# Optimization experiments

Hardware: AMD Instinct MI355X
Metric: run time of the kernel (lower is better)

Reference implementation:

```python
import jax, jax.numpy as jnp
import numpy as np

B, T, D = 2, 1024, 2048      # batch, seq, model dim
E, F, K = 64, 512, 4          # n_experts, expert hidden, top-k
S, HS = 2, 512 * 4            # shared experts, shared hidden = expert_dim * topk


def setup_inputs() -> dict:
    key = jax.random.key(0)
    ks = jax.random.split(key, 9)
    s = 0.02
    f32 = jnp.float32
    return {
        "x": jax.random.normal(ks[0], (B, T, D), f32),
        "router_w": jax.random.normal(ks[1], (D, E), f32) * s,
        "router_bias": jnp.zeros((E,), f32),
        "wg": jax.random.normal(ks[2], (E, D, F), f32) * s,
        "wu": jax.random.normal(ks[3], (E, D, F), f32) * s,
        "wd": jax.random.normal(ks[4], (E, F, D), f32) * s,
        "swg": jax.random.normal(ks[5], (S, D, HS), f32) * s,
        "swu": jax.random.normal(ks[6], (S, D, HS), f32) * s,
        "swd": jax.random.normal(ks[7], (S, HS, D), f32) * s,
    }


def reference(x, router_w, router_bias, wg, wu, wd, swg, swu, swd):
    b, t, d = x.shape
    flat = x.reshape(b * t, d)                      # [N, D]
    n = flat.shape[0]

    # Router: softmax scores, top-k selection on (logits + bias)
    logits = flat @ router_w                         # [N, E]
    scores = jax.nn.softmax(logits, axis=-1)
    _, topk_idx = jax.lax.top_k(logits + router_bias, K)          # [N, K]
    topk_scores = jnp.take_along_axis(scores, topk_idx, axis=-1)  # [N, K]
    topk_scores = topk_scores / topk_scores.sum(axis=-1, keepdims=True)

    # Dense combine weights: w[n, e] = normalized score if expert e selected else 0
    comb = jnp.zeros((n, E), dtype=flat.dtype).at[
        jnp.arange(n)[:, None], topk_idx].set(topk_scores)        # [N, E]

    # Routed experts (SwiGLU), computed densely and masked by combine weights
    g = jax.nn.silu(jnp.einsum('nd,edf->nef', flat, wg))          # [N, E, F]
    u = jnp.einsum('nd,edf->nef', flat, wu)                       # [N, E, F]
    routed = jnp.einsum('ne,nef,efd->nd', comb, g * u, wd)        # [N, D]

    # Shared experts (always active, summed)
    sg = jax.nn.silu(jnp.einsum('nd,sdh->nsh', flat, swg))        # [N, S, HS]
    su = jnp.einsum('nd,sdh->nsh', flat, swu)
    shared = jnp.einsum('nsh,shd->nd', sg * su, swd)              # [N, D]

    return (routed + shared).reshape(b, t, d)
```

## Files before the change

kernel.cpp:

```cpp
#include <hip/hip_runtime.h>
#include <hip/hip_bf16.h>

typedef __bf16 bf16x8 __attribute__((ext_vector_type(8)));
typedef float f32x4 __attribute__((ext_vector_type(4)));
typedef unsigned short u16x4 __attribute__((ext_vector_type(4)));
typedef unsigned short u16x8 __attribute__((ext_vector_type(8)));

#define DEVI __device__ __forceinline__

constexpr int N_TOK = 2048;
constexpr int DIM   = 2048;
constexpr int NEXP  = 64;
constexpr int FDIM  = 512;
constexpr int TOPK  = 4;
constexpr int NSH   = 2;
constexpr int HSH   = 2048;

constexpr int BM = 128, BN = 128, BK = 64, KS = 8;

DEVI unsigned short f2b(float f) {
  union { float fv; unsigned u; } v; v.fv = f;
  unsigned r = v.u + 0x7fffu + ((v.u >> 16) & 1u);
  return (unsigned short)(r >> 16);
}
DEVI float b2f(unsigned short h) {
  union { unsigned u; float f; } v; v.u = ((unsigned)h) << 16;
  return v.f;
}
DEVI void gll16(const void* g, void* l) {
  __builtin_amdgcn_global_load_lds((const __attribute__((address_space(1))) unsigned*)g,
                                   (__attribute__((address_space(3))) unsigned*)l, 16, 0, 0);
}

__global__ void cvt_x_kernel(const float* __restrict__ x, unsigned short* __restrict__ xb) {
  const size_t i = ((size_t)blockIdx.x * 256 + threadIdx.x) * 8;
  const float4 a = *reinterpret_cast<const float4*>(x + i);
  const float4 b = *reinterpret_cast<const float4*>(x + i + 4);
  u16x8 o;
  o[0] = f2b(a.x); o[1] = f2b(a.y); o[2] = f2b(a.z); o[3] = f2b(a.w);
  o[4] = f2b(b.x); o[5] = f2b(b.y); o[6] = f2b(b.z); o[7] = f2b(b.w);
  *reinterpret_cast<u16x8*>(xb + i) = o;
}

__global__ __launch_bounds__(256)
void tr_shared_kernel(const float* __restrict__ swu, const float* __restrict__ swg,
                      const float* __restrict__ swd, unsigned short* __restrict__ swuT,
                      unsigned short* __restrict__ swgT, unsigned short* __restrict__ swdT) {
  __shared__ float Lf[64][68];
  const int tid = threadIdx.x;
  const int r0 = blockIdx.x * 64, c0 = blockIdx.y * 64;
  const int z = blockIdx.z, mat = z >> 1;
  const size_t soff = (size_t)(z & 1) * DIM * HSH;
  const float* in = (mat == 0 ? swu : mat == 1 ? swg : swd) + soff;
  unsigned short* ot = (mat == 0 ? swuT : mat == 1 ? swgT : swdT) + soff;
  #pragma unroll
  for (int j = 0; j < 4; ++j) {
    const int idx = j * 1024 + tid * 4;
    const int row = idx >> 6, col = idx & 63;
    const float4 v = *reinterpret_cast<const float4*>(in + (size_t)(r0 + row) * 2048 + c0 + col);
    *reinterpret_cast<float4*>(&Lf[row][col]) = v;
  }
  __syncthreads();
  #pragma unroll
  for (int j = 0; j < 4; ++j) {
    const int idx = j * 1024 + tid * 4;
    const int orow = idx >> 6, ocol = idx & 63;
    u16x4 o;
    o[0] = f2b(Lf[ocol][orow]);     o[1] = f2b(Lf[ocol + 1][orow]);
    o[2] = f2b(Lf[ocol + 2][orow]); o[3] = f2b(Lf[ocol + 3][orow]);
    *reinterpret_cast<u16x4*>(ot + (size_t)(c0 + orow) * 2048 + r0 + ocol) = o;
  }
}

__global__ void router_kernel(const float* __restrict__ x, const float* __restrict__ rw,
                              const float* __restrict__ rb, int* __restrict__ cnt,
                              int* __restrict__ listTok, float* __restrict__ listW) {
  const int lane = threadIdx.x & 63;
  const int wave = threadIdx.x >> 6;
  const int tokBase = blockIdx.x * 8 + wave * 2;
  const float* __restrict__ xr0 = x + (size_t)tokBase * DIM;
  const float* __restrict__ xr1 = xr0 + DIM;
  float acc0 = 0.f, acc1 = 0.f;
  for (int d = 0; d < DIM; ++d) {
    const float r = rw[(size_t)d * NEXP + lane];
    acc0 = fmaf(xr0[d], r, acc0);
    acc1 = fmaf(xr1[d], r, acc1);
  }
  const float bias = rb[lane];
  #pragma unroll
  for (int t = 0; t < 2; ++t) {
    const float v = (t == 0) ? acc0 : acc1;
    const int token = tokBase + t;
    float m = v;
    #pragma unroll
    for (int o = 32; o > 0; o >>= 1) m = fmaxf(m, __shfl_xor(m, o));
    const float p = expf(v - m);
    float ss = p;
    #pragma unroll
    for (int o = 32; o > 0; o >>= 1) ss += __shfl_xor(ss, o);
    const float score = p / ss;
    float cur = v + bias;
    float wk[TOPK]; int ik[TOPK]; float wsum = 0.f;
    #pragma unroll
    for (int k = 0; k < TOPK; ++k) {
      float tm = cur;
      #pragma unroll
      for (int o = 32; o > 0; o >>= 1) tm = fmaxf(tm, __shfl_xor(tm, o));
      const unsigned long long msk = __ballot(cur == tm);
      const int sel = (int)__builtin_ctzll(msk);
      const float w = __shfl(score, sel);
      wk[k] = w; ik[k] = sel; wsum += w;
      if (lane == sel) cur = -3.4e38f;
    }
    if (lane < TOPK) {
      const int e = ik[lane];
      const float w = wk[lane] / wsum;
      const int slot = atomicAdd(&cnt[e], 1);
      listTok[(size_t)e * N_TOK + slot] = token;
      listW[(size_t)e * N_TOK + slot] = w;
    }
  }
}

__global__ void scan_kernel(const int* __restrict__ cnt, int* __restrict__ off) {
  if (threadIdx.x == 0) {
    int s = 0;
    for (int e = 0; e < NEXP; ++e) { off[e] = s; s += cnt[e]; }
  }
}

template<bool ROUTED>
__global__ __launch_bounds__(256, 2)
void up_fused_kernel(const unsigned short* __restrict__ xb,
                     const float* __restrict__ Wu, const float* __restrict__ Wg,
                     const unsigned short* __restrict__ WuT, const unsigned short* __restrict__ WgT,
                     const int* __restrict__ cnt, const int* __restrict__ off,
                     const int* __restrict__ listTok, const float* __restrict__ listW,
                     unsigned short* __restrict__ H) {
  const int Ftot = ROUTED ? FDIM : HSH;
  const int tid = threadIdx.x;
  const int f0 = blockIdx.x * BN;
  const int e  = blockIdx.y;
  const int m0 = blockIdx.z * BM;
  int rcnt, rowbase;
  if (ROUTED) {
    const int c = cnt[e];
    if (m0 >= c) return;
    rcnt = min(BM, c - m0);
    rowbase = off[e] + m0;
  } else {
    rcnt = BM;
    rowbase = e * N_TOK + m0;
  }

  __shared__ __align__(16) unsigned short Al[KS][BM][8];
  __shared__ __align__(16) unsigned short Bu[KS][BN][8];
  __shared__ __align__(16) unsigned short Bg[KS][BN][8];
  __shared__ int tokS[BM];
  __shared__ float wS[BM];

  if (tid < BM) {
    if (ROUTED) {
      const bool v = tid < rcnt;
      tokS[tid] = listTok[(size_t)e * N_TOK + m0 + (v ? tid : 0)];
      wS[tid]   = v ? listW[(size_t)e * N_TOK + m0 + tid] : 0.f;
    } else { tokS[tid] = m0 + tid; wS[tid] = 1.f; }
  }
  __syncthreads();

  const int wid = tid >> 6, l = tid & 63;
  const int wm = wid >> 1, wn = wid & 1;
  const int lc = l & 15, hi = l >> 4;

  const unsigned short* pa0 = xb + (size_t)tokS[l] * DIM;
  const unsigned short* pa1 = xb + (size_t)tokS[64 + l] * DIM;

  const unsigned short *pbu0 = nullptr, *pbu1 = nullptr, *pbg0 = nullptr, *pbg1 = nullptr;
  if constexpr (!ROUTED) {
    const unsigned short* wut = WuT + (size_t)e * HSH * DIM;
    const unsigned short* wgt = WgT + (size_t)e * HSH * DIM;
    pbu0 = wut + (size_t)(f0 + l) * DIM;  pbu1 = wut + (size_t)(f0 + 64 + l) * DIM;
    pbg0 = wgt + (size_t)(f0 + l) * DIM;  pbg1 = wgt + (size_t)(f0 + 64 + l) * DIM;
  }
  const int bf = tid & 127, kh = tid >> 7;
  const float *wpu = nullptr, *wpg = nullptr;
  if constexpr (ROUTED) {
    wpu = Wu + (size_t)e * DIM * FDIM + (size_t)(kh * 32) * FDIM + f0 + bf;
    wpg = Wg + (size_t)e * DIM * FDIM + (size_t)(kh * 32) * FDIM + f0 + bf;
  }
  unsigned short* bdstU = &Bu[kh * 4][bf][0];
  unsigned short* bdstG = &Bg[kh * 4][bf][0];

  f32x4 au[4][4], ag[4][4];
  #pragma unroll
  for (int i = 0; i < 4; ++i)
    #pragma unroll
    for (int j = 0; j < 4; ++j) { au[i][j] = f32x4{0,0,0,0}; ag[i][j] = f32x4{0,0,0,0}; }

  for (int d0 = 0; d0 < DIM; d0 += BK) {
    gll16(pa0 + d0 + (2 * wid) * 8,     &Al[2 * wid][0][0]);
    gll16(pa1 + d0 + (2 * wid) * 8,     &Al[2 * wid][64][0]);
    gll16(pa0 + d0 + (2 * wid + 1) * 8, &Al[2 * wid + 1][0][0]);
    gll16(pa1 + d0 + (2 * wid + 1) * 8, &Al[2 * wid + 1][64][0]);
    if constexpr (!ROUTED) {
      gll16(pbu0 + d0 + (2 * wid) * 8,     &Bu[2 * wid][0][0]);
      gll16(pbu1 + d0 + (2 * wid) * 8,     &Bu[2 * wid][64][0]);
      gll16(pbu0 + d0 + (2 * wid + 1) * 8, &Bu[2 * wid + 1][0][0]);
      gll16(pbu1 + d0 + (2 * wid + 1) * 8, &Bu[2 * wid + 1][64][0]);
      gll16(pbg0 + d0 + (2 * wid) * 8,     &Bg[2 * wid][0][0]);
      gll16(pbg1 + d0 + (2 * wid) * 8,     &Bg[2 * wid][64][0]);
      gll16(pbg0 + d0 + (2 * wid + 1) * 8, &Bg[2 * wid + 1][0][0]);
      gll16(pbg1 + d0 + (2 * wid + 1) * 8, &Bg[2 * wid + 1][64][0]);
    } else {
      float r[32];
      #pragma unroll
      for (int j = 0; j < 32; ++j) r[j] = wpu[(size_t)(d0 + j) * FDIM];
      #pragma unroll
      for (int jg = 0; jg < 4; ++jg) {
        u16x8 pk;
        #pragma unroll
        for (int q = 0; q < 8; ++q) pk[q] = f2b(r[jg * 8 + q]);
        *reinterpret_cast<u16x8*>(bdstU + jg * BN * 8) = pk;
      }
      #pragma unroll
      for (int j = 0; j < 32; ++j) r[j] = wpg[(size_t)(d0 + j) * FDIM];
      #pragma unroll
      for (int jg = 0; jg < 4; ++jg) {
        u16x8 pk;
        #pragma unroll
        for (int q = 0; q < 8; ++q) pk[q] = f2b(r[jg * 8 + q]);
        *reinterpret_cast<u16x8*>(bdstG + jg * BN * 8) = pk;
      }
    }
    __syncthreads();
    #pragma unroll
    for (int ks = 0; ks < 2; ++ks) {
      bf16x8 af[4], bu_[4], bg_[4];
      #pragma unroll
      for (int i = 0; i < 4; ++i)
        af[i] = *reinterpret_cast<const bf16x8*>(&Al[ks * 4 + hi][wm * 64 + i * 16 + lc][0]);
      #pragma unroll
      for (int i = 0; i < 4; ++i) {
        bu_[i] = *reinterpret_cast<const bf16x8*>(&Bu[ks * 4 + hi][wn * 64 + i * 16 + lc][0]);
        bg_[i] = *reinterpret_cast<const bf16x8*>(&Bg[ks * 4 + hi][wn * 64 + i * 16 + lc][0]);
      }
      #pragma unroll
      for (int mi = 0; mi < 4; ++mi)
        #pragma unroll
        for (int ni = 0; ni < 4; ++ni) {
          au[mi][ni] = __builtin_amdgcn_mfma_f32_16x16x32_bf16(af[mi], bu_[ni], au[mi][ni], 0, 0, 0);
          ag[mi][ni] = __builtin_amdgcn_mfma_f32_16x16x32_bf16(af[mi], bg_[ni], ag[mi][ni], 0, 0, 0);
        }
    }
    __syncthreads();
  }

  #pragma unroll
  for (int mi = 0; mi < 4; ++mi)
    #pragma unroll
    for (int ni = 0; ni < 4; ++ni)
      #pragma unroll
      for (int r2 = 0; r2 < 4; ++r2) {
        const int row = wm * 64 + mi * 16 + hi * 4 + r2;
        if (row < rcnt) {
          const int col = f0 + wn * 64 + ni * 16 + lc;
          const float g = ag[mi][ni][r2], u = au[mi][ni][r2];
          const float h = (g / (1.f + __expf(-g))) * u * wS[row];
          H[(size_t)(rowbase + row) * Ftot + col] = f2b(h);
        }
      }
}

__global__ __launch_bounds__(256, 2)
void down_kernel(const unsigned short* __restrict__ Hr, const unsigned short* __restrict__ Hs,
                 const float* __restrict__ wd, const unsigned short* __restrict__ swdT,
                 const int* __restrict__ cnt, const int* __restrict__ off,
                 const int* __restrict__ listTok, float* __restrict__ out) {
  const int tid = threadIdx.x;
  const int x0 = blockIdx.x * BN;
  const int y  = blockIdx.y;
  const int m0 = blockIdx.z * BM;
  const bool routed = y < NEXP;
  int rcnt, Kd;
  const unsigned short* Ab;
  const float* wb = nullptr;
  const unsigned short* wbT = nullptr;

  __shared__ int tokS[BM];
  __shared__ __align__(16) unsigned short Al[KS][BM][8];
  __shared__ __align__(16) unsigned short Bl[KS][BN][8];

  if (routed) {
    const int c = cnt[y];
    if (m0 >= c) return;
    rcnt = min(BM, c - m0); Kd = FDIM;
    Ab = Hr + (size_t)(off[y] + m0) * FDIM;
    wb = wd + (size_t)y * FDIM * DIM;
    if (tid < BM) tokS[tid] = listTok[(size_t)y * N_TOK + m0 + min(tid, rcnt - 1)];
  } else {
    const int s = y - NEXP;
    rcnt = BM; Kd = HSH;
    Ab = Hs + ((size_t)s * N_TOK + m0) * HSH;
    wbT = swdT + (size_t)s * HSH * DIM;
    if (tid < BM) tokS[tid] = m0 + tid;
  }
  __syncthreads();

  const int wid = tid >> 6, l = tid & 63;
  const int wm = wid >> 1, wn = wid & 1;
  const int lc = l & 15, hi = l >> 4;

  const unsigned short* pA = Ab + (size_t)l * Kd;
  const unsigned short *pBT0 = nullptr, *pBT1 = nullptr;
  if (!routed) {
    pBT0 = wbT + (size_t)(x0 + l) * HSH;
    pBT1 = wbT + (size_t)(x0 + 64 + l) * HSH;
  }
  const int bf = tid & 127, kh = tid >> 7;
  const float* wp = routed ? wb + (size_t)(kh * 32) * DIM + x0 + bf : nullptr;
  unsigned short* bdst = &Bl[kh * 4][bf][0];

  f32x4 acc[4][4];
  #pragma unroll
  for (int i = 0; i < 4; ++i)
    #pragma unroll
    for (int j = 0; j < 4; ++j) acc[i][j] = f32x4{0,0,0,0};

  for (int d0 = 0; d0 < Kd; d0 += BK) {
    gll16(pA + d0 + (2 * wid) * 8,                       &Al[2 * wid][0][0]);
    gll16(pA + (size_t)64 * Kd + d0 + (2 * wid) * 8,     &Al[2 * wid][64][0]);
    gll16(pA + d0 + (2 * wid + 1) * 8,                   &Al[2 * wid + 1][0][0]);
    gll16(pA + (size_t)64 * Kd + d0 + (2 * wid + 1) * 8, &Al[2 * wid + 1][64][0]);
    if (routed) {
      float r[32];
      #pragma unroll
      for (int j = 0; j < 32; ++j) r[j] = wp[(size_t)(d0 + j) * DIM];
      #pragma unroll
      for (int jg = 0; jg < 4; ++jg) {
        u16x8 pk;
        #pragma unroll
        for (int q = 0; q < 8; ++q) pk[q] = f2b(r[jg * 8 + q]);
        *reinterpret_cast<u16x8*>(bdst + jg * BN * 8) = pk;
      }
    } else {
      gll16(pBT0 + d0 + (2 * wid) * 8,     &Bl[2 * wid][0][0]);
      gll16(pBT1 + d0 + (2 * wid) * 8,     &Bl[2 * wid][64][0]);
      gll16(pBT0 + d0 + (2 * wid + 1) * 8, &Bl[2 * wid + 1][0][0]);
      gll16(pBT1 + d0 + (2 * wid + 1) * 8, &Bl[2 * wid + 1][64][0]);
    }
    __syncthreads();
    #pragma unroll
    for (int ks = 0; ks < 2; ++ks) {
      bf16x8 af[4], bq[4];
      #pragma unroll
      for (int i = 0; i < 4; ++i)
        af[i] = *reinterpret_cast<const bf16x8*>(&Al[ks * 4 + hi][wm * 64 + i * 16 + lc][0]);
      #pragma unroll
      for (int i = 0; i < 4; ++i)
        bq[i] = *reinterpret_cast<const bf16x8*>(&Bl[ks * 4 + hi][wn * 64 + i * 16 + lc][0]);
      #pragma unroll
      for (int mi = 0; mi < 4; ++mi)
        #pragma unroll
        for (int ni = 0; ni < 4; ++ni)
          acc[mi][ni] = __builtin_amdgcn_mfma_f32_16x16x32_bf16(af[mi], bq[ni], acc[mi][ni], 0, 0, 0);
    }
    __syncthreads();
  }

  #pragma unroll
  for (int mi = 0; mi < 4; ++mi)
    #pragma unroll
    for (int ni = 0; ni < 4; ++ni)
      #pragma unroll
      for (int r2 = 0; r2 < 4; ++r2) {
        const int row = wm * 64 + mi * 16 + hi * 4 + r2;
        if (row < rcnt) {
          const int col = x0 + wn * 64 + ni * 16 + lc;
          atomicAdd(&out[(size_t)tokS[row] * DIM + col], acc[mi][ni][r2]);
        }
      }
}

extern "C" void kernel_launch(void* const* d_in, const int* in_sizes, int n_in,
                              void* d_out, int out_size, void* d_ws, size_t ws_size,
                              hipStream_t stream) {
  const float* x   = (const float*)d_in[0];
  const float* rw  = (const float*)d_in[1];
  const float* rb  = (const float*)d_in[2];
  const float* wg  = (const float*)d_in[3];
  const float* wu  = (const float*)d_in[4];
  const float* wd  = (const float*)d_in[5];
  const float* swg = (const float*)d_in[6];
  const float* swu = (const float*)d_in[7];
  const float* swd = (const float*)d_in[8];
  float* out = (float*)d_out;
  char* ws = (char*)d_ws;

  int* cnt = (int*)ws;
  int* off = (int*)(ws + 256);
  int* listTok = (int*)(ws + 4096);
  float* listW = (float*)(ws + 4096 + 512 * 1024);
  unsigned short* xb   = (unsigned short*)(ws + (size_t) 2 * 1024 * 1024);
  unsigned short* Hr   = (unsigned short*)(ws + (size_t)10 * 1024 * 1024);
  unsigned short* Hs   = (unsigned short*)(ws + (size_t)18 * 1024 * 1024);
  unsigned short* swuT = (unsigned short*)(ws + (size_t)34 * 1024 * 1024);
  unsigned short* swgT = (unsigned short*)(ws + (size_t)50 * 1024 * 1024);
  unsigned short* swdT = (unsigned short*)(ws + (size_t)66 * 1024 * 1024);

  hipMemsetAsync(cnt, 0, NEXP * sizeof(int), stream);
  hipMemsetAsync(out, 0, (size_t)N_TOK * DIM * sizeof(float), stream);
  cvt_x_kernel<<<(N_TOK * DIM) / (256 * 8), 256, 0, stream>>>(x, xb);
  tr_shared_kernel<<<dim3(32, 32, 6), 256, 0, stream>>>(swu, swg, swd, swuT, swgT, swdT);
  router_kernel<<<N_TOK / 8, 256, 0, stream>>>(x, rw, rb, cnt, listTok, listW);
  scan_kernel<<<1, 64, 0, stream>>>(cnt, off);
  up_fused_kernel<true ><<<dim3(FDIM / BN, NEXP, 16), 256, 0, stream>>>(
      xb, wu, wg, nullptr, nullptr, cnt, off, listTok, listW, Hr);
  up_fused_kernel<false><<<dim3(HSH / BN, NSH, N_TOK / BM), 256, 0, stream>>>(
      xb, nullptr, nullptr, swuT, swgT, cnt, off, listTok, listW, Hs);
  down_kernel<<<dim3(DIM / BN, NEXP + NSH, 16), 256, 0, stream>>>(
      Hr, Hs, wd, swdT, cnt, off, listTok, out);
}
```

Measured before the change: 693.4 us.

## Split routed up-projection into two passes, vectorize fp32 weight loads, tile router input

The routed up-projection now runs as two passes: the first computes the up projection and stores it to H in bf16, the second computes the gate projection and fuses SiLU, the multiply and the routing weight into its epilogue. Splitting cuts the accumulator count in half, which eases register pressure, but the token activations are reloaded and H is written and read an extra time. The fp32 expert weights are now fetched as float4 loads along F and transposed into LDS as packed bf16, replacing scalar strided loads, in both the up and down kernels. The shared up kernel uses 64-wide N tiles to keep two accumulator sets within the register budget, and the router stages x in LDS in 128-column chunks.

```diff
diff --git a/kernel.cpp b/kernel.cpp
--- a/kernel.cpp
+++ b/kernel.cpp
@@ -16,7 +16,7 @@
 constexpr int NSH   = 2;
 constexpr int HSH   = 2048;
 
-constexpr int BM = 128, BN = 128, BK = 64, KS = 8;
+constexpr int BK = 64, KS = 8;
 
 DEVI unsigned short f2b(float f) {
   union { float fv; unsigned u; } v; v.fv = f;
@@ -72,25 +72,39 @@
   }
 }
 
-__global__ void router_kernel(const float* __restrict__ x, const float* __restrict__ rw,
-                              const float* __restrict__ rb, int* __restrict__ cnt,
-                              int* __restrict__ listTok, float* __restrict__ listW) {
-  const int lane = threadIdx.x & 63;
-  const int wave = threadIdx.x >> 6;
-  const int tokBase = blockIdx.x * 8 + wave * 2;
-  const float* __restrict__ xr0 = x + (size_t)tokBase * DIM;
-  const float* __restrict__ xr1 = xr0 + DIM;
+__global__ __launch_bounds__(256)
+void router_kernel(const float* __restrict__ x, const float* __restrict__ rw,
+                   const float* __restrict__ rb, int* __restrict__ cnt,
+                   int* __restrict__ listTok, float* __restrict__ listW) {
+  __shared__ float Lx[8][128];
+  const int tid = threadIdx.x;
+  const int lane = tid & 63;
+  const int wave = tid >> 6;
+  const int tokBase = blockIdx.x * 8;
+
   float acc0 = 0.f, acc1 = 0.f;
-  for (int d = 0; d < DIM; ++d) {
-    const float r = rw[(size_t)d * NEXP + lane];
-    acc0 = fmaf(xr0[d], r, acc0);
-    acc1 = fmaf(xr1[d], r, acc1);
-  }
+  for (int dc = 0; dc < DIM; dc += 128) {
+    __syncthreads();
+    {
+      const int idx = tid * 4;
+      const int row = idx >> 7, col = idx & 127;
+      *reinterpret_cast<float4*>(&Lx[row][col]) =
+          *reinterpret_cast<const float4*>(x + (size_t)(tokBase + row) * DIM + dc + col);
+    }
+    __syncthreads();
+    #pragma unroll 16
+    for (int dd = 0; dd < 128; ++dd) {
+      const float r = rw[(size_t)(dc + dd) * NEXP + lane];
+      acc0 = fmaf(Lx[wave * 2 + 0][dd], r, acc0);
+      acc1 = fmaf(Lx[wave * 2 + 1][dd], r, acc1);
+    }
+  }
+
   const float bias = rb[lane];
   #pragma unroll
   for (int t = 0; t < 2; ++t) {
     const float v = (t == 0) ? acc0 : acc1;
-    const int token = tokBase + t;
+    const int token = tokBase + wave * 2 + t;
     float m = v;
     #pragma unroll
     for (int o = 32; o > 0; o >>= 1) m = fmaxf(m, __shfl_xor(m, o));
@@ -129,42 +143,29 @@
   }
 }
 
-template<bool ROUTED>
+template<bool GPASS>
 __global__ __launch_bounds__(256, 2)
-void up_fused_kernel(const unsigned short* __restrict__ xb,
-                     const float* __restrict__ Wu, const float* __restrict__ Wg,
-                     const unsigned short* __restrict__ WuT, const unsigned short* __restrict__ WgT,
-                     const int* __restrict__ cnt, const int* __restrict__ off,
-                     const int* __restrict__ listTok, const float* __restrict__ listW,
-                     unsigned short* __restrict__ H) {
-  const int Ftot = ROUTED ? FDIM : HSH;
+void up_routed(const unsigned short* __restrict__ xb, const float* __restrict__ W,
+               const int* __restrict__ cnt, const int* __restrict__ off,
+               const int* __restrict__ listTok, const float* __restrict__ listW,
+               unsigned short* __restrict__ H) {
   const int tid = threadIdx.x;
-  const int f0 = blockIdx.x * BN;
+  const int f0 = blockIdx.x * 128;
   const int e  = blockIdx.y;
-  const int m0 = blockIdx.z * BM;
-  int rcnt, rowbase;
-  if (ROUTED) {
-    const int c = cnt[e];
-    if (m0 >= c) return;
-    rcnt = min(BM, c - m0);
-    rowbase = off[e] + m0;
-  } else {
-    rcnt = BM;
-    rowbase = e * N_TOK + m0;
-  }
-
-  __shared__ __align__(16) unsigned short Al[KS][BM][8];
-  __shared__ __align__(16) unsigned short Bu[KS][BN][8];
-  __shared__ __align__(16) unsigned short Bg[KS][BN][8];
-  __shared__ int tokS[BM];
-  __shared__ float wS[BM];
-
-  if (tid < BM) {
-    if (ROUTED) {
-      const bool v = tid < rcnt;
-      tokS[tid] = listTok[(size_t)e * N_TOK + m0 + (v ? tid : 0)];
-      wS[tid]   = v ? listW[(size_t)e * N_TOK + m0 + tid] : 0.f;
-    } else { tokS[tid] = m0 + tid; wS[tid] = 1.f; }
+  const int m0 = blockIdx.z * 128;
+  const int c = cnt[e];
+  if (m0 >= c) return;
+  const int rcnt = min(128, c - m0);
+  const int rowbase = off[e] + m0;
+
+  __shared__ __align__(16) unsigned short Al[KS][128][8];
+  __shared__ __align__(16) unsigned short Bl[KS][128][8];
+  __shared__ int tokS[128];
+  __shared__ float wS[128];
+
+  if (tid < 128) {
+    tokS[tid] = listTok[(size_t)e * N_TOK + m0 + min(tid, rcnt - 1)];
+    wS[tid] = (tid < rcnt) ? listW[(size_t)e * N_TOK + m0 + tid] : 0.f;
   }
   __syncthreads();
 
@@ -174,83 +175,51 @@
 
   const unsigned short* pa0 = xb + (size_t)tokS[l] * DIM;
   const unsigned short* pa1 = xb + (size_t)tokS[64 + l] * DIM;
-
-  const unsigned short *pbu0 = nullptr, *pbu1 = nullptr, *pbg0 = nullptr, *pbg1 = nullptr;
-  if constexpr (!ROUTED) {
-    const unsigned short* wut = WuT + (size_t)e * HSH * DIM;
-    const unsigned short* wgt = WgT + (size_t)e * HSH * DIM;
-    pbu0 = wut + (size_t)(f0 + l) * DIM;  pbu1 = wut + (size_t)(f0 + 64 + l) * DIM;
-    pbg0 = wgt + (size_t)(f0 + l) * DIM;  pbg1 = wgt + (size_t)(f0 + 64 + l) * DIM;
-  }
-  const int bf = tid & 127, kh = tid >> 7;
-  const float *wpu = nullptr, *wpg = nullptr;
-  if constexpr (ROUTED) {
-    wpu = Wu + (size_t)e * DIM * FDIM + (size_t)(kh * 32) * FDIM + f0 + bf;
-    wpg = Wg + (size_t)e * DIM * FDIM + (size_t)(kh * 32) * FDIM + f0 + bf;
-  }
-  unsigned short* bdstU = &Bu[kh * 4][bf][0];
-  unsigned short* bdstG = &Bg[kh * 4][bf][0];
-
-  f32x4 au[4][4], ag[4][4];
+  const float* bw = W + (size_t)e * DIM * FDIM + f0;
+  const int f4 = tid & 31, k4a = tid >> 5;
+
+  f32x4 acc[4][4];
   #pragma unroll
   for (int i = 0; i < 4; ++i)
     #pragma unroll
-    for (int j = 0; j < 4; ++j) { au[i][j] = f32x4{0,0,0,0}; ag[i][j] = f32x4{0,0,0,0}; }
+    for (int j = 0; j < 4; ++j) acc[i][j] = f32x4{0.f, 0.f, 0.f, 0.f};
 
   for (int d0 = 0; d0 < DIM; d0 += BK) {
     gll16(pa0 + d0 + (2 * wid) * 8,     &Al[2 * wid][0][0]);
     gll16(pa1 + d0 + (2 * wid) * 8,     &Al[2 * wid][64][0]);
     gll16(pa0 + d0 + (2 * wid + 1) * 8, &Al[2 * wid + 1][0][0]);
     gll16(pa1 + d0 + (2 * wid + 1) * 8, &Al[2 * wid + 1][64][0]);
-    if constexpr (!ROUTED) {
-      gll16(pbu0 + d0 + (2 * wid) * 8,     &Bu[2 * wid][0][0]);
-      gll16(pbu1 + d0 + (2 * wid) * 8,     &Bu[2 * wid][64][0]);
-      gll16(pbu0 + d0 + (2 * wid + 1) * 8, &Bu[2 * wid + 1][0][0]);
-      gll16(pbu1 + d0 + (2 * wid + 1) * 8, &Bu[2 * wid + 1][64][0]);
-      gll16(pbg0 + d0 + (2 * wid) * 8,     &Bg[2 * wid][0][0]);
-      gll16(pbg1 + d0 + (2 * wid) * 8,     &Bg[2 * wid][64][0]);
-      gll16(pbg0 + d0 + (2 * wid + 1) * 8, &Bg[2 * wid + 1][0][0]);
-      gll16(pbg1 + d0 + (2 * wid + 1) * 8, &Bg[2 * wid + 1][64][0]);
-    } else {
-      float r[32];
-      #pragma unroll
-      for (int j = 0; j < 32; ++j) r[j] = wpu[(size_t)(d0 + j) * FDIM];
-      #pragma unroll
-      for (int jg = 0; jg < 4; ++jg) {
-        u16x8 pk;
-        #pragma unroll
-        for (int q = 0; q < 8; ++q) pk[q] = f2b(r[jg * 8 + q]);
-        *reinterpret_cast<u16x8*>(bdstU + jg * BN * 8) = pk;
-      }
-      #pragma unroll
-      for (int j = 0; j < 32; ++j) r[j] = wpg[(size_t)(d0 + j) * FDIM];
-      #pragma unroll
-      for (int jg = 0; jg < 4; ++jg) {
-        u16x8 pk;
-        #pragma unroll
-        for (int q = 0; q < 8; ++q) pk[q] = f2b(r[jg * 8 + q]);
-        *reinterpret_cast<u16x8*>(bdstG + jg * BN * 8) = pk;
-      }
+    f32x4 rB[2][4];
+    #pragma unroll
+    for (int s2 = 0; s2 < 2; ++s2)
+      #pragma unroll
+      for (int j = 0; j < 4; ++j)
+        rB[s2][j] = *reinterpret_cast<const f32x4*>(
+            bw + (size_t)(d0 + k4a * 8 + s2 * 4 + j) * FDIM + f4 * 4);
+    #pragma unroll
+    for (int cc = 0; cc < 4; ++cc) {
+      u16x8 v;
+      v[0] = f2b(rB[0][0][cc]); v[1] = f2b(rB[0][1][cc]);
+      v[2] = f2b(rB[0][2][cc]); v[3] = f2b(rB[0][3][cc]);
+      v[4] = f2b(rB[1][0][cc]); v[5] = f2b(rB[1][1][cc]);
+      v[6] = f2b(rB[1][2][cc]); v[7] = f2b(rB[1][3][cc]);
+      *reinterpret_cast<u16x8*>(&Bl[k4a][f4 * 4 + cc][0]) = v;
     }
     __syncthreads();
     #pragma unroll
     for (int ks = 0; ks < 2; ++ks) {
-      bf16x8 af[4], bu_[4], bg_[4];
+      bf16x8 af[4], bq[4];
       #pragma unroll
       for (int i = 0; i < 4; ++i)
         af[i] = *reinterpret_cast<const bf16x8*>(&Al[ks * 4 + hi][wm * 64 + i * 16 + lc][0]);
       #pragma unroll
-      for (int i = 0; i < 4; ++i) {
-        bu_[i] = *reinterpret_cast<const bf16x8*>(&Bu[ks * 4 + hi][wn * 64 + i * 16 + lc][0]);
-        bg_[i] = *reinterpret_cast<const bf16x8*>(&Bg[ks * 4 + hi][wn * 64 + i * 16 + lc][0]);
-      }
+      for (int i = 0; i < 4; ++i)
+        bq[i] = *reinterpret_cast<const bf16x8*>(&Bl[ks * 4 + hi][wn * 64 + i * 16 + lc][0]);
       #pragma unroll
       for (int mi = 0; mi < 4; ++mi)
         #pragma unroll
-        for (int ni = 0; ni < 4; ++ni) {
-          au[mi][ni] = __builtin_amdgcn_mfma_f32_16x16x32_bf16(af[mi], bu_[ni], au[mi][ni], 0, 0, 0);
-          ag[mi][ni] = __builtin_amdgcn_mfma_f32_16x16x32_bf16(af[mi], bg_[ni], ag[mi][ni], 0, 0, 0);
-        }
+        for (int ni = 0; ni < 4; ++ni)
+          acc[mi][ni] = __builtin_amdgcn_mfma_f32_16x16x32_bf16(af[mi], bq[ni], acc[mi][ni], 0, 0, 0);
     }
     __syncthreads();
   }
@@ -264,89 +233,170 @@
         const int row = wm * 64 + mi * 16 + hi * 4 + r2;
         if (row < rcnt) {
           const int col = f0 + wn * 64 + ni * 16 + lc;
-          const float g = ag[mi][ni][r2], u = au[mi][ni][r2];
-          const float h = (g / (1.f + __expf(-g))) * u * wS[row];
-          H[(size_t)(rowbase + row) * Ftot + col] = f2b(h);
+          const size_t idx = (size_t)(rowbase + row) * FDIM + col;
+          const float v = acc[mi][ni][r2];
+          if constexpr (GPASS) {
+            const float u = b2f(H[idx]);
+            H[idx] = f2b((v / (1.f + __expf(-v))) * u * wS[row]);
+          } else {
+            H[idx] = f2b(v);
+          }
         }
       }
 }
 
 __global__ __launch_bounds__(256, 2)
-void down_kernel(const unsigned short* __restrict__ Hr, const unsigned short* __restrict__ Hs,
-                 const float* __restrict__ wd, const unsigned short* __restrict__ swdT,
-                 const int* __restrict__ cnt, const int* __restrict__ off,
-                 const int* __restrict__ listTok, float* __restrict__ out) {
+void up_shared(const unsigned short* __restrict__ xb,
+               const unsigned short* __restrict__ WuT, const unsigned short* __restrict__ WgT,
+               unsigned short* __restrict__ H) {
   const int tid = threadIdx.x;
-  const int x0 = blockIdx.x * BN;
+  const int f0 = blockIdx.x * 64;
+  const int s  = blockIdx.y;
+  const int m0 = blockIdx.z * 128;
+
+  __shared__ __align__(16) unsigned short Al[KS][128][8];
+  __shared__ __align__(16) unsigned short Bu[KS][64][8];
+  __shared__ __align__(16) unsigned short Bg[KS][64][8];
+
+  const int wid = tid >> 6, l = tid & 63;
+  const int wm = wid >> 1, wn = wid & 1;
+  const int lc = l & 15, hi = l >> 4;
+
+  const unsigned short* pa0 = xb + (size_t)(m0 + l) * DIM;
+  const unsigned short* pa1 = xb + (size_t)(m0 + 64 + l) * DIM;
+  const unsigned short* pbu = WuT + (size_t)s * HSH * DIM + (size_t)(f0 + l) * DIM;
+  const unsigned short* pbg = WgT + (size_t)s * HSH * DIM + (size_t)(f0 + l) * DIM;
+
+  f32x4 aU[4][2], aG[4][2];
+  #pragma unroll
+  for (int i = 0; i < 4; ++i)
+    #pragma unroll
+    for (int j = 0; j < 2; ++j) { aU[i][j] = f32x4{0.f,0.f,0.f,0.f}; aG[i][j] = f32x4{0.f,0.f,0.f,0.f}; }
+
+  for (int d0 = 0; d0 < DIM; d0 += BK) {
+    gll16(pa0 + d0 + (2 * wid) * 8,     &Al[2 * wid][0][0]);
+    gll16(pa1 + d0 + (2 * wid) * 8,     &Al[2 * wid][64][0]);
+    gll16(pa0 + d0 + (2 * wid + 1) * 8, &Al[2 * wid + 1][0][0]);
+    gll16(pa1 + d0 + (2 * wid + 1) * 8, &Al[2 * wid + 1][64][0]);
+    gll16(pbu + d0 + (2 * wid) * 8,     &Bu[2 * wid][0][0]);
+    gll16(pbu + d0 + (2 * wid + 1) * 8, &Bu[2 * wid + 1][0][0]);
+    gll16(pbg + d0 + (2 * wid) * 8,     &Bg[2 * wid][0][0]);
+    gll16(pbg + d0 + (2 * wid + 1) * 8, &Bg[2 * wid + 1][0][0]);
+    __syncthreads();
+    #pragma unroll
+    for (int ks = 0; ks < 2; ++ks) {
+      bf16x8 af[4], bu[2], bg[2];
+      #pragma unroll
+      for (int i = 0; i < 4; ++i)
+        af[i] = *reinterpret_cast<const bf16x8*>(&Al[ks * 4 + hi][wm * 64 + i * 16 + lc][0]);
+      #pragma unroll
+      for (int i = 0; i < 2; ++i) {
+        bu[i] = *reinterpret_cast<const bf16x8*>(&Bu[ks * 4 + hi][wn * 32 + i * 16 + lc][0]);
+        bg[i] = *reinterpret_cast<const bf16x8*>(&Bg[ks * 4 + hi][wn * 32 + i * 16 + lc][0]);
+      }
+      #pragma unroll
+      for (int mi = 0; mi < 4; ++mi)
+        #pragma unroll
+        for (int ni = 0; ni < 2; ++ni) {
+          aU[mi][ni] = __builtin_amdgcn_mfma_f32_16x16x32_bf16(af[mi], bu[ni], aU[mi][ni], 0, 0, 0);
+          aG[mi][ni] = __builtin_amdgcn_mfma_f32_16x16x32_bf16(af[mi], bg[ni], aG[mi][ni], 0, 0, 0);
+        }
+    }
+    __syncthreads();
+  }
+
+  #pragma unroll
+  for (int mi = 0; mi < 4; ++mi)
+    #pragma unroll
+    for (int ni = 0; ni < 2; ++ni)
+      #pragma unroll
+      for (int r2 = 0; r2 < 4; ++r2) {
+        const int row = wm * 64 + mi * 16 + hi * 4 + r2;
+        const int col = f0 + wn * 32 + ni * 16 + lc;
+        const float g = aG[mi][ni][r2], u = aU[mi][ni][r2];
+        const float h = (g / (1.f + __expf(-g))) * u;
+        H[((size_t)s * N_TOK + m0 + row) * HSH + col] = f2b(h);
+      }
+}
+
+__global__ __launch_bounds__(256, 2)
+void down_all(const unsigned short* __restrict__ Hr, const unsigned short* __restrict__ Hs,
+              const float* __restrict__ wd, const unsigned short* __restrict__ swdT,
+              const int* __restrict__ cnt, const int* __restrict__ off,
+              const int* __restrict__ listTok, float* __restrict__ out) {
+  const int tid = threadIdx.x;
+  const int x0 = blockIdx.x * 128;
   const int y  = blockIdx.y;
-  const int m0 = blockIdx.z * BM;
+  const int m0 = blockIdx.z * 128;
   const bool routed = y < NEXP;
-  int rcnt, Kd;
-  const unsigned short* Ab;
-  const float* wb = nullptr;
-  const unsigned short* wbT = nullptr;
-
-  __shared__ int tokS[BM];
-  __shared__ __align__(16) unsigned short Al[KS][BM][8];
-  __shared__ __align__(16) unsigned short Bl[KS][BN][8];
+
+  __shared__ __align__(16) unsigned short Al[KS][128][8];
+  __shared__ __align__(16) unsigned short Bl[KS][128][8];
+  __shared__ int tokS[128];
+
+  const int wid = tid >> 6, l = tid & 63;
+  const int wm = wid >> 1, wn = wid & 1;
+  const int lc = l & 15, hi = l >> 4;
+
+  int rcnt = 128, Kd;
+  const unsigned short *pa0, *pa1, *pb0 = nullptr, *pb1 = nullptr;
+  const float* bw = nullptr;
 
   if (routed) {
     const int c = cnt[y];
     if (m0 >= c) return;
-    rcnt = min(BM, c - m0); Kd = FDIM;
-    Ab = Hr + (size_t)(off[y] + m0) * FDIM;
-    wb = wd + (size_t)y * FDIM * DIM;
-    if (tid < BM) tokS[tid] = listTok[(size_t)y * N_TOK + m0 + min(tid, rcnt - 1)];
+    rcnt = min(128, c - m0);
+    const int rowbase = off[y] + m0;
+    Kd = FDIM;
+    if (tid < 128) tokS[tid] = listTok[(size_t)y * N_TOK + m0 + min(tid, rcnt - 1)];
+    pa0 = Hr + (size_t)(rowbase + min(l, rcnt - 1)) * FDIM;
+    pa1 = Hr + (size_t)(rowbase + min(64 + l, rcnt - 1)) * FDIM;
+    bw = wd + (size_t)y * FDIM * DIM + x0;
   } else {
     const int s = y - NEXP;
-    rcnt = BM; Kd = HSH;
-    Ab = Hs + ((size_t)s * N_TOK + m0) * HSH;
-    wbT = swdT + (size_t)s * HSH * DIM;
-    if (tid < BM) tokS[tid] = m0 + tid;
-  }
-  __syncthreads();
-
-  const int wid = tid >> 6, l = tid & 63;
-  const int wm = wid >> 1, wn = wid & 1;
-  const int lc = l & 15, hi = l >> 4;
-
-  const unsigned short* pA = Ab + (size_t)l * Kd;
-  const unsigned short *pBT0 = nullptr, *pBT1 = nullptr;
-  if (!routed) {
-    pBT0 = wbT + (size_t)(x0 + l) * HSH;
-    pBT1 = wbT + (size_t)(x0 + 64 + l) * HSH;
-  }
-  const int bf = tid & 127, kh = tid >> 7;
-  const float* wp = routed ? wb + (size_t)(kh * 32) * DIM + x0 + bf : nullptr;
-  unsigned short* bdst = &Bl[kh * 4][bf][0];
+    Kd = HSH;
+    if (tid < 128) tokS[tid] = m0 + tid;
+    pa0 = Hs + ((size_t)s * N_TOK + m0 + l) * HSH;
+    pa1 = Hs + ((size_t)s * N_TOK + m0 + 64 + l) * HSH;
+    pb0 = swdT + (size_t)s * HSH * DIM + (size_t)(x0 + l) * HSH;
+    pb1 = swdT + (size_t)s * HSH * DIM + (size_t)(x0 + 64 + l) * HSH;
+  }
+
+  const int f4 = tid & 31, k4a = tid >> 5;
 
   f32x4 acc[4][4];
   #pragma unroll
   for (int i = 0; i < 4; ++i)
     #pragma unroll
-    for (int j = 0; j < 4; ++j) acc[i][j] = f32x4{0,0,0,0};
+    for (int j = 0; j < 4; ++j) acc[i][j] = f32x4{0.f, 0.f, 0.f, 0.f};
 
   for (int d0 = 0; d0 < Kd; d0 += BK) {
-    gll16(pA + d0 + (2 * wid) * 8,                       &Al[2 * wid][0][0]);
-    gll16(pA + (size_t)64 * Kd + d0 + (2 * wid) * 8,     &Al[2 * wid][64][0]);
-    gll16(pA + d0 + (2 * wid + 1) * 8,                   &Al[2 * wid + 1][0][0]);
-    gll16(pA + (size_t)64 * Kd + d0 + (2 * wid + 1) * 8, &Al[2 * wid + 1][64][0]);
+    gll16(pa0 + d0 + (2 * wid) * 8,     &Al[2 * wid][0][0]);
+    gll16(pa1 + d0 + (2 * wid) * 8,     &Al[2 * wid][64][0]);
+    gll16(pa0 + d0 + (2 * wid + 1) * 8, &Al[2 * wid + 1][0][0]);
+    gll16(pa1 + d0 + (2 * wid + 1) * 8, &Al[2 * wid + 1][64][0]);
     if (routed) {
-      float r[32];
-      #pragma unroll
-      for (int j = 0; j < 32; ++j) r[j] = wp[(size_t)(d0 + j) * DIM];
-      #pragma unroll
-      for (int jg = 0; jg < 4; ++jg) {
-        u16x8 pk;
+      f32x4 rB[2][4];
+      #pragma unroll
+      for (int s2 = 0; s2 < 2; ++s2)
         #pragma unroll
-        for (int q = 0; q < 8; ++q) pk[q] = f2b(r[jg * 8 + q]);
-        *reinterpret_cast<u16x8*>(bdst + jg * BN * 8) = pk;
+        for (int j = 0; j < 4; ++j)
+          rB[s2][j] = *reinterpret_cast<const f32x4*>(
+              bw + (size_t)(d0 + k4a * 8 + s2 * 4 + j) * DIM + f4 * 4);
+      #pragma unroll
+      for (int cc = 0; cc < 4; ++cc) {
+        u16x8 v;
+        v[0] = f2b(rB[0][0][cc]); v[1] = f2b(rB[0][1][cc]);
+        v[2] = f2b(rB[0][2][cc]); v[3] = f2b(rB[0][3][cc]);
+        v[4] = f2b(rB[1][0][cc]); v[5] = f2b(rB[1][1][cc]);
+        v[6] = f2b(rB[1][2][cc]); v[7] = f2b(rB[1][3][cc]);
+        *reinterpret_cast<u16x8*>(&Bl[k4a][f4 * 4 + cc][0]) = v;
       }
     } else {
-      gll16(pBT0 + d0 + (2 * wid) * 8,     &Bl[2 * wid][0][0]);
-      gll16(pBT1 + d0 + (2 * wid) * 8,     &Bl[2 * wid][64][0]);
-      gll16(pBT0 + d0 + (2 * wid + 1) * 8, &Bl[2 * wid + 1][0][0]);
-      gll16(pBT1 + d0 + (2 * wid + 1) * 8, &Bl[2 * wid + 1][64][0]);
+      gll16(pb0 + d0 + (2 * wid) * 8,     &Bl[2 * wid][0][0]);
+      gll16(pb1 + d0 + (2 * wid) * 8,     &Bl[2 * wid][64][0]);
+      gll16(pb0 + d0 + (2 * wid + 1) * 8, &Bl[2 * wid + 1][0][0]);
+      gll16(pb1 + d0 + (2 * wid + 1) * 8, &Bl[2 * wid + 1][64][0]);
     }
     __syncthreads();
     #pragma unroll
@@ -413,10 +463,13 @@
   tr_shared_kernel<<<dim3(32, 32, 6), 256, 0, stream>>>(swu, swg, swd, swuT, swgT, swdT);
   router_kernel<<<N_TOK / 8, 256, 0, stream>>>(x, rw, rb, cnt, listTok, listW);
   scan_kernel<<<1, 64, 0, stream>>>(cnt, off);
-  up_fused_kernel<true ><<<dim3(FDIM / BN, NEXP, 16), 256, 0, stream>>>(
-      xb, wu, wg, nullptr, nullptr, cnt, off, listTok, listW, Hr);
-  up_fused_kernel<false><<<dim3(HSH / BN, NSH, N_TOK / BM), 256, 0, stream>>>(
-      xb, nullptr, nullptr, swuT, swgT, cnt, off, listTok, listW, Hs);
-  down_kernel<<<dim3(DIM / BN, NEXP + NSH, 16), 256, 0, stream>>>(
+
+  up_routed<false><<<dim3(FDIM / 128, NEXP, 16), 256, 0, stream>>>(
+      xb, wu, cnt, off, listTok, listW, Hr);
+  up_routed<true><<<dim3(FDIM / 128, NEXP, 16), 256, 0, stream>>>(
+      xb, wg, cnt, off, listTok, listW, Hr);
+  up_shared<<<dim3(HSH / 64, NSH, N_TOK / 128), 256, 0, stream>>>(
+      xb, swuT, swgT, Hs);
+  down_all<<<dim3(DIM / 128, NEXP + NSH, 16), 256, 0, stream>>>(
       Hr, Hs, wd, swdT, cnt, off, listTok, out);
 }
```

New measurement: 687.6 us. No clear change (-0.8%).
